# Optimization experiments

Measured on AMD Instinct MI355X. Metric: run time of the kernel, lower is better.

The kernel has to match this reference:

```python
import jax, jax.numpy as jnp
import numpy as np

N_USERS = 100000
M_ITEMS = 50000
D = 64
NNZ = 4_000_000
B = 4096
LAYERS = 3


def setup_inputs() -> dict:
    key = jax.random.key(0)
    ks = jax.random.split(key, 7)
    N = N_USERS + M_ITEMS
    return {
        "users": jax.random.randint(ks[0], (B,), 0, N_USERS, dtype=jnp.int64 if jax.config.jax_enable_x64 else jnp.int32),
        "items": jax.random.randint(ks[1], (B,), 0, M_ITEMS, dtype=jnp.int64 if jax.config.jax_enable_x64 else jnp.int32),
        "user_emb": jax.random.normal(ks[2], (N_USERS, D), dtype=jnp.float32) * 0.1,
        "item_emb": jax.random.normal(ks[3], (M_ITEMS, D), dtype=jnp.float32) * 0.1,
        "adj_rows": jax.random.randint(ks[4], (NNZ,), 0, N, dtype=jnp.int32),
        "adj_cols": jax.random.randint(ks[5], (NNZ,), 0, N, dtype=jnp.int32),
        "adj_vals": jax.random.uniform(ks[6], (NNZ,), dtype=jnp.float32),
    }


def reference(users, items, user_emb, item_emb, adj_rows, adj_cols, adj_vals):
    n_users = user_emb.shape[0]
    N = n_users + item_emb.shape[0]

    # computer(): multi-layer sparse propagation, mean over layer outputs
    all_emb = jnp.concatenate([user_emb, item_emb], axis=0)  # [N, D]
    acc = all_emb
    emb = all_emb
    for _ in range(LAYERS):
        # SpMM as gather + segment-sum: (A @ emb)[r] = sum_{e: row(e)=r} val(e) * emb[col(e)]
        messages = adj_vals[:, None] * emb[adj_cols]          # [NNZ, D]
        emb = jax.ops.segment_sum(messages, adj_rows, num_segments=N)
        acc = acc + emb
    light_out = acc / (LAYERS + 1)                            # mean over stacked layers

    all_users = light_out[:n_users]
    all_items = light_out[n_users:]

    # forward(users, items)
    u = all_users[users]                                      # [B, D]
    i = all_items[items]                                      # [B, D]
    gamma = jnp.sum(u * i, axis=1)                            # [B]
    return gamma
```

## Files before the change

### kernel.cpp

```cpp
#include <hip/hip_runtime.h>

#define N_USERS 100000
#define M_ITEMS 50000
#define N_TOTAL (N_USERS + M_ITEMS)
#define D 64
#define NNZ 4000000
#define BATCH 4096

#define RPB 128
#define BSHIFT 7
#define NBUCKETS ((N_TOTAL + RPB - 1) / RPB)
#define BCAP 7680

#define TILE 8192
#define SCAT_BLOCKS ((NNZ + TILE - 1) / TILE)
#define SCAT_THREADS 1024
#define EPT (TILE / SCAT_THREADS)
#define CPB 2

#define LS_THREADS 1024
#define LS_EPT 8

typedef __attribute__((ext_vector_type(2))) float f32x2;
typedef __attribute__((ext_vector_type(2))) int   i32x2;

__device__ __forceinline__ unsigned pack_bf16(float a, float b) {
    unsigned ua = __float_as_uint(a);
    unsigned ub = __float_as_uint(b);
    ua = (ua + 0x7FFFu + ((ua >> 16) & 1u)) >> 16;
    ub = (ub + 0x7FFFu + ((ub >> 16) & 1u)) & 0xFFFF0000u;
    return ua | ub;
}
__device__ __forceinline__ float bf16_lo(unsigned p) { return __uint_as_float(p << 16); }
__device__ __forceinline__ float bf16_hi(unsigned p) { return __uint_as_float(p & 0xFFFF0000u); }

__device__ __forceinline__ f32x2 unpack_bf16x2(unsigned p) {
    union { unsigned u[2]; f32x2 f; } r;
    r.u[0] = p << 16;
    r.u[1] = p & 0xFFFF0000u;
    return r.f;
}


__global__ void init_emb_kernel(const float4* __restrict__ ue,
                                const float4* __restrict__ ie,
                                uint2* __restrict__ emb) {
    size_t i = (size_t)blockIdx.x * blockDim.x + threadIdx.x;
    const size_t nu4  = (size_t)N_USERS * D / 4;
    const size_t tot4 = (size_t)N_TOTAL * D / 4;
    if (i >= tot4) return;
    float4 f = (i < nu4) ? ue[i] : ie[i - nu4];
    emb[i] = make_uint2(pack_bf16(f.x, f.y), pack_bf16(f.z, f.w));
}


__global__ void bucket_hist_kernel(const int* __restrict__ rows,
                                   int* __restrict__ bucketcnt) {
    __shared__ int h[NBUCKETS];
    for (int i = threadIdx.x; i < NBUCKETS; i += blockDim.x) h[i] = 0;
    __syncthreads();
    int stride = gridDim.x * blockDim.x;
    for (int e = blockIdx.x * blockDim.x + threadIdx.x; e < NNZ; e += stride)
        atomicAdd(&h[__builtin_nontemporal_load(rows + e) >> BSHIFT], 1);
    __syncthreads();
    for (int i = threadIdx.x; i < NBUCKETS; i += blockDim.x)
        if (h[i]) atomicAdd(&bucketcnt[i], h[i]);
}

__global__ void bucket_scan_kernel(const int* __restrict__ cnt,
                                   int* __restrict__ bucketoff,
                                   int* __restrict__ cursor) {
    __shared__ int sc[1024];
    int t = threadIdx.x;
    int i0 = t * 2, i1 = t * 2 + 1;
    int a = (i0 < NBUCKETS) ? cnt[i0] : 0;
    int b = (i1 < NBUCKETS) ? cnt[i1] : 0;
    sc[t] = a + b;
    __syncthreads();
    for (int o = 1; o < 1024; o <<= 1) {
        int v = (t >= o) ? sc[t - o] : 0;
        __syncthreads();
        sc[t] += v;
        __syncthreads();
    }
    int excl = (t == 0) ? 0 : sc[t - 1];
    if (i0 < NBUCKETS) { bucketoff[i0] = excl;     cursor[i0] = excl; }
    if (i1 < NBUCKETS) { bucketoff[i1] = excl + a; cursor[i1] = excl + a; }
    if (t == 0) bucketoff[NBUCKETS] = NNZ;
}

__global__ __launch_bounds__(SCAT_THREADS)
void bucket_scatter_kernel(const int* __restrict__ rows,
                           const int* __restrict__ cols,
                           const float* __restrict__ vals,
                           int* __restrict__ cursor,
                           int2* __restrict__ bucketed) {
    __shared__ int hist[NBUCKETS];
    __shared__ int loff[NBUCKETS + 1];
    __shared__ int partial[SCAT_THREADS];
    __shared__ int2 buf[TILE];
    __shared__ int dst[TILE];
    int t = threadIdx.x;
    size_t start = (size_t)blockIdx.x * TILE;
    int n = (int)(((size_t)NNZ - start < TILE) ? ((size_t)NNZ - start) : TILE);

    for (int i = t; i < NBUCKETS; i += SCAT_THREADS) hist[i] = 0;
    __syncthreads();
    int rowv[EPT];
    int rank[EPT];
#pragma unroll
    for (int k = 0; k < EPT; ++k) {
        int i = t + k * SCAT_THREADS;
        if (i < n) {
            int r = __builtin_nontemporal_load(rows + start + i);
            rowv[k] = r;
            rank[k] = atomicAdd(&hist[r >> BSHIFT], 1);
        }
    }
    __syncthreads();
    {
        int base = t * CPB;
        int s = 0;
#pragma unroll
        for (int j = 0; j < CPB; ++j) {
            int idx = base + j;
            if (idx < NBUCKETS) s += hist[idx];
        }
        partial[t] = s;
        __syncthreads();
        for (int o = 1; o < SCAT_THREADS; o <<= 1) {
            int v = (t >= o) ? partial[t - o] : 0;
            __syncthreads();
            partial[t] += v;
            __syncthreads();
        }
        int excl = (t == 0) ? 0 : partial[t - 1];
#pragma unroll
        for (int j = 0; j < CPB; ++j) {
            int idx = base + j;
            if (idx < NBUCKETS) { loff[idx] = excl; excl += hist[idx]; }
        }
        if (t == 0) loff[NBUCKETS] = n;
    }
    __syncthreads();
    for (int i = t; i < NBUCKETS; i += SCAT_THREADS) {
        int c = loff[i + 1] - loff[i];
        hist[i] = c ? atomicAdd(&cursor[i], c) : 0;
    }
    __syncthreads();
#pragma unroll
    for (int k = 0; k < EPT; ++k) {
        int i = t + k * SCAT_THREADS;
        if (i < n) {
            int r = rowv[k];
            int bkt = r >> BSHIFT;
            int slot = loff[bkt] + rank[k];
            int cv = __builtin_nontemporal_load(cols + start + i);
            float vv = __builtin_nontemporal_load(vals + start + i);
            buf[slot] = make_int2(((r & (RPB - 1)) << 18) | cv, __float_as_int(vv));
            dst[slot] = hist[bkt] + rank[k];
        }
    }
    __syncthreads();
    for (int i = t; i < n; i += SCAT_THREADS)
        bucketed[dst[i]] = buf[i];
}

__global__ __launch_bounds__(LS_THREADS)
void local_sort_kernel(const int* __restrict__ bucketoff,
                       const int2* __restrict__ bucketed,
                       int* __restrict__ row_start,
                       int2* __restrict__ edges) {
    __shared__ int hist[RPB];
    __shared__ int sc[RPB];
    __shared__ int2 buf[BCAP];
    int b = blockIdx.x;
    int t = threadIdx.x;
    int s = bucketoff[b], e = bucketoff[b + 1], n = e - s;

    if (t < RPB) hist[t] = 0;
    __syncthreads();
    int rl[LS_EPT], rank[LS_EPT];
    int2 pay[LS_EPT];
#pragma unroll
    for (int k = 0; k < LS_EPT; ++k) {
        int i = t + k * LS_THREADS;
        if (i < n) {
            i32x2 ev = __builtin_nontemporal_load((const i32x2*)(bucketed + s + i));
            rl[k] = (int)((unsigned)ev.x >> 18);
            pay[k] = make_int2((ev.x & 0x3FFFF) << 7, ev.y);
            rank[k] = atomicAdd(&hist[rl[k]], 1);
        }
    }
    __syncthreads();
    if (t < RPB) sc[t] = hist[t];
    __syncthreads();
    for (int o = 1; o < RPB; o <<= 1) {
        int v = (t < RPB && t >= o) ? sc[t - o] : 0;
        __syncthreads();
        if (t < RPB) sc[t] += v;
        __syncthreads();
    }
    if (t < RPB) {
        int excl = (t == 0) ? 0 : sc[t - 1];
        int gr = b * RPB + t;
        if (gr < N_TOTAL) row_start[gr] = s + excl;
    }
    if (b == 0 && t == 0) row_start[N_TOTAL] = NNZ;
    __syncthreads();
#pragma unroll
    for (int k = 0; k < LS_EPT; ++k) {
        int i = t + k * LS_THREADS;
        if (i < n) {
            int excl = (rl[k] == 0) ? 0 : sc[rl[k] - 1];
            int p = excl + rank[k];
            if (p < BCAP) buf[p] = pay[k];
            else          edges[s + p] = pay[k];
        }
    }
    __syncthreads();
    int m = (n < BCAP) ? n : BCAP;
    for (int i = t; i < m; i += LS_THREADS) edges[s + i] = buf[i];
}


#define EDGE_LD(p_) __builtin_nontemporal_load((const i32x2*)(p_))

#define EDGE_SLOT(ei, ji)                                                    \
    {                                                                        \
        int   c_  = (ji < n) ? ei.x : 0;                                     \
        float mv_ = (ji < n) ? __int_as_float(ei.y) : 0.0f;                  \
        uint4 p_  = *(const uint4*)(ebase + c_);                             \
        f32x2 vv_ = {mv_, mv_};                                              \
        a01 = __builtin_elementwise_fma(unpack_bf16x2(p_.x), vv_, a01);      \
        a23 = __builtin_elementwise_fma(unpack_bf16x2(p_.y), vv_, a23);      \
        a45 = __builtin_elementwise_fma(unpack_bf16x2(p_.z), vv_, a45);      \
        a67 = __builtin_elementwise_fma(unpack_bf16x2(p_.w), vv_, a67);      \
    }

#define SPMM_BODY(row_s, row_e)                                              \
    int n = (row_e) - (row_s);                                               \
    const int2* ep = edges + (row_s) + oct;                                  \
    f32x2 a01 = {0.f, 0.f}, a23 = {0.f, 0.f};                                \
    f32x2 a45 = {0.f, 0.f}, a67 = {0.f, 0.f};                                \
    int tmax = (n + 7) >> 3;                                                 \
    int t = 0;                                                               \
    for (; t + 4 <= tmax; t += 4) {                                          \
        i32x2 e0 = EDGE_LD(ep), e1 = EDGE_LD(ep + 8);                        \
        i32x2 e2 = EDGE_LD(ep + 16), e3 = EDGE_LD(ep + 24);                  \
        ep += 32;                                                            \
        int j0 = (t << 3) + oct;                                             \
        EDGE_SLOT(e0, j0);                                                   \
        EDGE_SLOT(e1, (j0 + 8));                                             \
        EDGE_SLOT(e2, (j0 + 16));                                            \
        EDGE_SLOT(e3, (j0 + 24));                                            \
    }                                                                        \
    if (t + 2 <= tmax) {                                                     \
        i32x2 e0 = EDGE_LD(ep), e1 = EDGE_LD(ep + 8);                        \
        ep += 16;                                                            \
        int j0 = (t << 3) + oct;                                             \
        EDGE_SLOT(e0, j0);                                                   \
        EDGE_SLOT(e1, (j0 + 8));                                             \
        t += 2;                                                              \
    }                                                                        \
    if (t < tmax) {                                                          \
        i32x2 e0 = EDGE_LD(ep);                                              \
        int j0 = (t << 3) + oct;                                             \
        EDGE_SLOT(e0, j0);                                                   \
    }                                                                        \
    _Pragma("unroll")                                                        \
    for (int o = 8; o <= 32; o <<= 1) {                                      \
        a01.x += __shfl_xor(a01.x, o, 64); a01.y += __shfl_xor(a01.y, o, 64);\
        a23.x += __shfl_xor(a23.x, o, 64); a23.y += __shfl_xor(a23.y, o, 64);\
        a45.x += __shfl_xor(a45.x, o, 64); a45.y += __shfl_xor(a45.y, o, 64);\
        a67.x += __shfl_xor(a67.x, o, 64); a67.y += __shfl_xor(a67.y, o, 64);\
    }

__global__ void spmm_csr_kernel(const int* __restrict__ row_start,
                                const int2* __restrict__ edges,
                                const char* __restrict__ emb_in,
                                uint4* __restrict__ emb_out) {
    int wave = (blockIdx.x * blockDim.x + threadIdx.x) >> 6;
    int lane = threadIdx.x & 63;
    if (wave >= N_TOTAL) return;
    int oct = lane >> 3;
    int ui  = lane & 7;
    const char* ebase = emb_in + (ui << 4);
    int s = row_start[wave];
    int e = row_start[wave + 1];
    SPMM_BODY(s, e);
    if (oct == 0)
        emb_out[(size_t)wave * 8 + ui] =
            make_uint4(pack_bf16(a01.x, a01.y), pack_bf16(a23.x, a23.y),
                       pack_bf16(a45.x, a45.y), pack_bf16(a67.x, a67.y));
}

__global__ void finalize_kernel(const int* __restrict__ users,
                                const int* __restrict__ items,
                                const float* __restrict__ ue,
                                const float* __restrict__ ie,
                                const int* __restrict__ row_start,
                                const int2* __restrict__ edges,
                                const char* __restrict__ embB,
                                const char* __restrict__ embA,
                                float* __restrict__ out) {
    int wave = (blockIdx.x * blockDim.x + threadIdx.x) >> 6;
    int lane = threadIdx.x & 63;
    if (wave >= BATCH) return;
    int oct = lane >> 3;
    int ui  = lane & 7;
    const char* ebase = embA + (ui << 4);

    int ru = users[wave];
    int ri = N_USERS + items[wave];

    f32x2 u01, u23, u45, u67, i01, i23, i45, i67;
    {
        SPMM_BODY(row_start[ru], row_start[ru + 1]);
        u01 = a01; u23 = a23; u45 = a45; u67 = a67;
    }
    {
        SPMM_BODY(row_start[ri], row_start[ri + 1]);
        i01 = a01; i23 = a23; i45 = a45; i67 = a67;
    }

    {
        const float4* up = (const float4*)(ue + (size_t)ru * D + 8 * ui);
        float4 f0 = up[0], f1 = up[1];
        u01 += (f32x2){f0.x, f0.y}; u23 += (f32x2){f0.z, f0.w};
        u45 += (f32x2){f1.x, f1.y}; u67 += (f32x2){f1.z, f1.w};
        uint4 pb = *(const uint4*)(embB + (size_t)ru * 128 + (ui << 4));
        uint4 pa = *(const uint4*)(embA + (size_t)ru * 128 + (ui << 4));
        u01 += unpack_bf16x2(pb.x) + unpack_bf16x2(pa.x);
        u23 += unpack_bf16x2(pb.y) + unpack_bf16x2(pa.y);
        u45 += unpack_bf16x2(pb.z) + unpack_bf16x2(pa.z);
        u67 += unpack_bf16x2(pb.w) + unpack_bf16x2(pa.w);
    }
    {
        const float4* ip = (const float4*)(ie + (size_t)items[wave] * D + 8 * ui);
        float4 f0 = ip[0], f1 = ip[1];
        i01 += (f32x2){f0.x, f0.y}; i23 += (f32x2){f0.z, f0.w};
        i45 += (f32x2){f1.x, f1.y}; i67 += (f32x2){f1.z, f1.w};
        uint4 pb = *(const uint4*)(embB + (size_t)ri * 128 + (ui << 4));
        uint4 pa = *(const uint4*)(embA + (size_t)ri * 128 + (ui << 4));
        i01 += unpack_bf16x2(pb.x) + unpack_bf16x2(pa.x);
        i23 += unpack_bf16x2(pb.y) + unpack_bf16x2(pa.y);
        i45 += unpack_bf16x2(pb.z) + unpack_bf16x2(pa.z);
        i67 += unpack_bf16x2(pb.w) + unpack_bf16x2(pa.w);
    }

    f32x2 d = u01 * i01;
    d = __builtin_elementwise_fma(u23, i23, d);
    d = __builtin_elementwise_fma(u45, i45, d);
    d = __builtin_elementwise_fma(u67, i67, d);
    float p = d.x + d.y;
#pragma unroll
    for (int o = 1; o <= 4; o <<= 1) p += __shfl_xor(p, o, 64);
    if (lane == 0) out[wave] = p * (1.0f / 16.0f);
}


extern "C" void kernel_launch(void* const* d_in, const int* in_sizes, int n_in,
                              void* d_out, int out_size, void* d_ws, size_t ws_size,
                              hipStream_t stream) {
    const int*   users = (const int*)d_in[0];
    const int*   items = (const int*)d_in[1];
    const float* ue    = (const float*)d_in[2];
    const float* ie    = (const float*)d_in[3];
    const int*   rows  = (const int*)d_in[4];
    const int*   cols  = (const int*)d_in[5];
    const float* vals  = (const float*)d_in[6];
    float*       out   = (float*)d_out;

    char* ws = (char*)d_ws;
    size_t off = 0;
    auto alloc = [&](size_t bytes) {
        void* p = ws + off;
        off += (bytes + 255) & ~(size_t)255;
        return p;
    };
    const size_t NBH = (size_t)N_TOTAL * D * sizeof(unsigned short);
    char*  embA      = (char*)alloc(NBH);
    char*  embB      = (char*)alloc(NBH);
    int*   row_start = (int*)alloc(((size_t)N_TOTAL + 1) * sizeof(int));
    int*   bucketcnt = (int*)alloc((size_t)NBUCKETS * sizeof(int));
    int*   bucketoff = (int*)alloc(((size_t)NBUCKETS + 1) * sizeof(int));
    int*   cursor    = (int*)alloc((size_t)NBUCKETS * sizeof(int));
    int2*  edges     = (int2*)alloc((size_t)NNZ * sizeof(int2) + 256);
    int2*  bucketed  = (int2*)alloc((size_t)NNZ * sizeof(int2));

    {
        size_t tot4 = (size_t)N_TOTAL * D / 4;
        init_emb_kernel<<<(unsigned)((tot4 + 255) / 256), 256, 0, stream>>>(
            (const float4*)ue, (const float4*)ie, (uint2*)embA);
    }

    hipMemsetAsync(bucketcnt, 0, (size_t)NBUCKETS * sizeof(int), stream);
    bucket_hist_kernel<<<512, 256, 0, stream>>>(rows, bucketcnt);
    bucket_scan_kernel<<<1, 1024, 0, stream>>>(bucketcnt, bucketoff, cursor);
    bucket_scatter_kernel<<<SCAT_BLOCKS, SCAT_THREADS, 0, stream>>>(
        rows, cols, vals, cursor, bucketed);
    local_sort_kernel<<<NBUCKETS, LS_THREADS, 0, stream>>>(
        bucketoff, bucketed, row_start, edges);

    spmm_csr_kernel<<<(N_TOTAL * 64 + 255) / 256, 256, 0, stream>>>(
        row_start, edges, embA, (uint4*)embB);

    spmm_csr_kernel<<<(N_TOTAL * 64 + 255) / 256, 256, 0, stream>>>(
        row_start, edges, embB, (uint4*)embA);

    finalize_kernel<<<(BATCH * 64 + 255) / 256, 256, 0, stream>>>(
        users, items, ue, ie, row_start, edges, embB, embA, out);
}
```

Measured before the change: 344.1 us.

## Sort edges within rows by column block to improve gather locality

The local sort now bins edges by (row, column>>12) rather than by row alone. Edges inside each row therefore come out ordered by coarse column block, which should improve cache locality of the embedding gathers in the SpMM. This needs a larger shared histogram and a 1024-wide block scan, and the shared staging buffer shrinks so more edges spill to direct global writes. The SpMM edge loads also switch from nontemporal loads to plain int2 loads.

```diff
diff --git a/kernel.cpp b/kernel.cpp
--- a/kernel.cpp
+++ b/kernel.cpp
@@ -10,7 +10,6 @@
 #define RPB 128
 #define BSHIFT 7
 #define NBUCKETS ((N_TOTAL + RPB - 1) / RPB)
-#define BCAP 7680
 
 #define TILE 8192
 #define SCAT_BLOCKS ((NNZ + TILE - 1) / TILE)
@@ -20,6 +19,11 @@
 
 #define LS_THREADS 1024
 #define LS_EPT 8
+#define CBSHIFT 12
+#define NCB 37
+#define NBINS (RPB * NCB)
+#define BPT ((NBINS + LS_THREADS - 1) / LS_THREADS)
+#define BCAP 4608
 
 typedef __attribute__((ext_vector_type(2))) float f32x2;
 typedef __attribute__((ext_vector_type(2))) int   i32x2;
@@ -31,8 +35,6 @@
     ub = (ub + 0x7FFFu + ((ub >> 16) & 1u)) & 0xFFFF0000u;
     return ua | ub;
 }
-__device__ __forceinline__ float bf16_lo(unsigned p) { return __uint_as_float(p << 16); }
-__device__ __forceinline__ float bf16_hi(unsigned p) { return __uint_as_float(p & 0xFFFF0000u); }
 
 __device__ __forceinline__ f32x2 unpack_bf16x2(unsigned p) {
     union { unsigned u[2]; f32x2 f; } r;
@@ -171,49 +173,65 @@
                        const int2* __restrict__ bucketed,
                        int* __restrict__ row_start,
                        int2* __restrict__ edges) {
-    __shared__ int hist[RPB];
-    __shared__ int sc[RPB];
+    __shared__ int hist[NBINS];
+    __shared__ int partial[LS_THREADS];
     __shared__ int2 buf[BCAP];
     int b = blockIdx.x;
     int t = threadIdx.x;
     int s = bucketoff[b], e = bucketoff[b + 1], n = e - s;
 
-    if (t < RPB) hist[t] = 0;
-    __syncthreads();
-    int rl[LS_EPT], rank[LS_EPT];
+    for (int i = t; i < NBINS; i += LS_THREADS) hist[i] = 0;
+    __syncthreads();
+    int binv[LS_EPT], rank[LS_EPT];
     int2 pay[LS_EPT];
 #pragma unroll
     for (int k = 0; k < LS_EPT; ++k) {
         int i = t + k * LS_THREADS;
         if (i < n) {
             i32x2 ev = __builtin_nontemporal_load((const i32x2*)(bucketed + s + i));
-            rl[k] = (int)((unsigned)ev.x >> 18);
-            pay[k] = make_int2((ev.x & 0x3FFFF) << 7, ev.y);
-            rank[k] = atomicAdd(&hist[rl[k]], 1);
-        }
-    }
-    __syncthreads();
-    if (t < RPB) sc[t] = hist[t];
-    __syncthreads();
-    for (int o = 1; o < RPB; o <<= 1) {
-        int v = (t < RPB && t >= o) ? sc[t - o] : 0;
+            int rl  = (int)((unsigned)ev.x >> 18);
+            int col = ev.x & 0x3FFFF;
+            binv[k] = rl * NCB + (col >> CBSHIFT);
+            pay[k] = make_int2(col << 7, ev.y);
+            rank[k] = atomicAdd(&hist[binv[k]], 1);
+        }
+    }
+    __syncthreads();
+    int loc[BPT];
+    {
+        int ssum = 0;
+#pragma unroll
+        for (int j = 0; j < BPT; ++j) {
+            int idx = t * BPT + j;
+            loc[j] = ssum;
+            if (idx < NBINS) ssum += hist[idx];
+        }
+        partial[t] = ssum;
         __syncthreads();
-        if (t < RPB) sc[t] += v;
-        __syncthreads();
-    }
+        for (int o = 1; o < LS_THREADS; o <<= 1) {
+            int v = (t >= o) ? partial[t - o] : 0;
+            __syncthreads();
+            partial[t] += v;
+            __syncthreads();
+        }
+        int excl = (t == 0) ? 0 : partial[t - 1];
+#pragma unroll
+        for (int j = 0; j < BPT; ++j) {
+            int idx = t * BPT + j;
+            if (idx < NBINS) hist[idx] = excl + loc[j];
+        }
+    }
+    __syncthreads();
     if (t < RPB) {
-        int excl = (t == 0) ? 0 : sc[t - 1];
         int gr = b * RPB + t;
-        if (gr < N_TOTAL) row_start[gr] = s + excl;
+        if (gr < N_TOTAL) row_start[gr] = s + hist[t * NCB];
     }
     if (b == 0 && t == 0) row_start[N_TOTAL] = NNZ;
-    __syncthreads();
 #pragma unroll
     for (int k = 0; k < LS_EPT; ++k) {
         int i = t + k * LS_THREADS;
         if (i < n) {
-            int excl = (rl[k] == 0) ? 0 : sc[rl[k] - 1];
-            int p = excl + rank[k];
+            int p = hist[binv[k]] + rank[k];
             if (p < BCAP) buf[p] = pay[k];
             else          edges[s + p] = pay[k];
         }
@@ -223,8 +241,6 @@
     for (int i = t; i < m; i += LS_THREADS) edges[s + i] = buf[i];
 }
 
-
-#define EDGE_LD(p_) __builtin_nontemporal_load((const i32x2*)(p_))
 
 #define EDGE_SLOT(ei, ji)                                                    \
     {                                                                        \
@@ -246,8 +262,7 @@
     int tmax = (n + 7) >> 3;                                                 \
     int t = 0;                                                               \
     for (; t + 4 <= tmax; t += 4) {                                          \
-        i32x2 e0 = EDGE_LD(ep), e1 = EDGE_LD(ep + 8);                        \
-        i32x2 e2 = EDGE_LD(ep + 16), e3 = EDGE_LD(ep + 24);                  \
+        int2 e0 = ep[0], e1 = ep[8], e2 = ep[16], e3 = ep[24];               \
         ep += 32;                                                            \
         int j0 = (t << 3) + oct;                                             \
         EDGE_SLOT(e0, j0);                                                   \
@@ -256,7 +271,7 @@
         EDGE_SLOT(e3, (j0 + 24));                                            \
     }                                                                        \
     if (t + 2 <= tmax) {                                                     \
-        i32x2 e0 = EDGE_LD(ep), e1 = EDGE_LD(ep + 8);                        \
+        int2 e0 = ep[0], e1 = ep[8];                                         \
         ep += 16;                                                            \
         int j0 = (t << 3) + oct;                                             \
         EDGE_SLOT(e0, j0);                                                   \
@@ -264,7 +279,7 @@
         t += 2;                                                              \
     }                                                                        \
     if (t < tmax) {                                                          \
-        i32x2 e0 = EDGE_LD(ep);                                              \
+        int2 e0 = ep[0];                                                     \
         int j0 = (t << 3) + oct;                                             \
         EDGE_SLOT(e0, j0);                                                   \
     }                                                                        \
```

Measured after the change: 345.9 us. About the same (+0.5%).

## Fuse first SpMM layer into local sort and merge init with histogram

Applied to the files above, without the earlier changes.

Runs the first propagation layer inside the per-bucket local sort kernel, reading edges from shared memory instead of reloading them from global memory, which saves one kernel launch and one pass over the edge array. Embedding init is merged with the bucket histogram into a single launch. Block scans now use wave shuffles instead of barrier-heavy shared-memory loops, and several output writes become nontemporal stores. The fused layer runs on only 16 waves per block of 128 rows, so it has less parallelism and latency hiding than the standalone SpMM kernel.

```diff
diff --git a/kernel.cpp b/kernel.cpp
--- a/kernel.cpp
+++ b/kernel.cpp
@@ -21,8 +21,26 @@
 #define LS_THREADS 1024
 #define LS_EPT 8
 
-typedef __attribute__((ext_vector_type(2))) float f32x2;
-typedef __attribute__((ext_vector_type(2))) int   i32x2;
+#define INIT_BLOCKS 9375
+#define HIST_BLOCKS 512
+
+typedef __attribute__((ext_vector_type(2))) float    f32x2;
+typedef __attribute__((ext_vector_type(2))) int      i32x2;
+typedef __attribute__((ext_vector_type(4))) unsigned u32x4;
+typedef __attribute__((ext_vector_type(2))) unsigned u32x2;
+
+__device__ __forceinline__ void nt_store_int2(int2 v, int2* p) {
+    i32x2 t; t.x = v.x; t.y = v.y;
+    __builtin_nontemporal_store(t, (i32x2*)p);
+}
+__device__ __forceinline__ void nt_store_uint4(uint4 v, uint4* p) {
+    u32x4 t; t.x = v.x; t.y = v.y; t.z = v.z; t.w = v.w;
+    __builtin_nontemporal_store(t, (u32x4*)p);
+}
+__device__ __forceinline__ void nt_store_uint2(uint2 v, uint2* p) {
+    u32x2 t; t.x = v.x; t.y = v.y;
+    __builtin_nontemporal_store(t, (u32x2*)p);
+}
 
 __device__ __forceinline__ unsigned pack_bf16(float a, float b) {
     unsigned ua = __float_as_uint(a);
@@ -31,8 +49,6 @@
     ub = (ub + 0x7FFFu + ((ub >> 16) & 1u)) & 0xFFFF0000u;
     return ua | ub;
 }
-__device__ __forceinline__ float bf16_lo(unsigned p) { return __uint_as_float(p << 16); }
-__device__ __forceinline__ float bf16_hi(unsigned p) { return __uint_as_float(p & 0xFFFF0000u); }
 
 __device__ __forceinline__ f32x2 unpack_bf16x2(unsigned p) {
     union { unsigned u[2]; f32x2 f; } r;
@@ -41,26 +57,47 @@
     return r.f;
 }
 
-
-__global__ void init_emb_kernel(const float4* __restrict__ ue,
-                                const float4* __restrict__ ie,
-                                uint2* __restrict__ emb) {
-    size_t i = (size_t)blockIdx.x * blockDim.x + threadIdx.x;
-    const size_t nu4  = (size_t)N_USERS * D / 4;
-    const size_t tot4 = (size_t)N_TOTAL * D / 4;
-    if (i >= tot4) return;
-    float4 f = (i < nu4) ? ue[i] : ie[i - nu4];
-    emb[i] = make_uint2(pack_bf16(f.x, f.y), pack_bf16(f.z, f.w));
-}
-
-
-__global__ void bucket_hist_kernel(const int* __restrict__ rows,
-                                   int* __restrict__ bucketcnt) {
+__device__ __forceinline__ int block_scan_incl_1024(int v, int* wsum) {
+    int lane = threadIdx.x & 63, wv = threadIdx.x >> 6;
+#pragma unroll
+    for (int o = 1; o < 64; o <<= 1) {
+        int u = __shfl_up(v, o, 64);
+        if (lane >= o) v += u;
+    }
+    if (lane == 63) wsum[wv] = v;
+    __syncthreads();
+    if (wv == 0) {
+        int w = (lane < 16) ? wsum[lane] : 0;
+#pragma unroll
+        for (int o = 1; o < 16; o <<= 1) {
+            int u = __shfl_up(w, o, 64);
+            if (lane >= o) w += u;
+        }
+        if (lane < 16) wsum[lane] = w;
+    }
+    __syncthreads();
+    return v + (wv ? wsum[wv - 1] : 0);
+}
+
+__global__ void init_hist_kernel(const float4* __restrict__ ue,
+                                 const float4* __restrict__ ie,
+                                 uint2* __restrict__ emb,
+                                 const int* __restrict__ rows,
+                                 int* __restrict__ bucketcnt) {
     __shared__ int h[NBUCKETS];
+    if (blockIdx.x < INIT_BLOCKS) {
+        size_t i = (size_t)blockIdx.x * 256 + threadIdx.x;
+        const size_t nu4 = (size_t)N_USERS * D / 4;
+        float4 f = (i < nu4) ? ue[i] : ie[i - nu4];
+        nt_store_uint2(make_uint2(pack_bf16(f.x, f.y), pack_bf16(f.z, f.w)),
+                       emb + i);
+        return;
+    }
+    int bid = blockIdx.x - INIT_BLOCKS;
     for (int i = threadIdx.x; i < NBUCKETS; i += blockDim.x) h[i] = 0;
     __syncthreads();
-    int stride = gridDim.x * blockDim.x;
-    for (int e = blockIdx.x * blockDim.x + threadIdx.x; e < NNZ; e += stride)
+    int stride = HIST_BLOCKS * 256;
+    for (int e = bid * 256 + threadIdx.x; e < NNZ; e += stride)
         atomicAdd(&h[__builtin_nontemporal_load(rows + e) >> BSHIFT], 1);
     __syncthreads();
     for (int i = threadIdx.x; i < NBUCKETS; i += blockDim.x)
@@ -70,20 +107,13 @@
 __global__ void bucket_scan_kernel(const int* __restrict__ cnt,
                                    int* __restrict__ bucketoff,
                                    int* __restrict__ cursor) {
-    __shared__ int sc[1024];
+    __shared__ int wsum[16];
     int t = threadIdx.x;
     int i0 = t * 2, i1 = t * 2 + 1;
     int a = (i0 < NBUCKETS) ? cnt[i0] : 0;
     int b = (i1 < NBUCKETS) ? cnt[i1] : 0;
-    sc[t] = a + b;
-    __syncthreads();
-    for (int o = 1; o < 1024; o <<= 1) {
-        int v = (t >= o) ? sc[t - o] : 0;
-        __syncthreads();
-        sc[t] += v;
-        __syncthreads();
-    }
-    int excl = (t == 0) ? 0 : sc[t - 1];
+    int incl = block_scan_incl_1024(a + b, wsum);
+    int excl = incl - a - b;
     if (i0 < NBUCKETS) { bucketoff[i0] = excl;     cursor[i0] = excl; }
     if (i1 < NBUCKETS) { bucketoff[i1] = excl + a; cursor[i1] = excl + a; }
     if (t == 0) bucketoff[NBUCKETS] = NNZ;
@@ -97,7 +127,7 @@
                            int2* __restrict__ bucketed) {
     __shared__ int hist[NBUCKETS];
     __shared__ int loff[NBUCKETS + 1];
-    __shared__ int partial[SCAT_THREADS];
+    __shared__ int wsum[16];
     __shared__ int2 buf[TILE];
     __shared__ int dst[TILE];
     int t = threadIdx.x;
@@ -126,15 +156,7 @@
             int idx = base + j;
             if (idx < NBUCKETS) s += hist[idx];
         }
-        partial[t] = s;
-        __syncthreads();
-        for (int o = 1; o < SCAT_THREADS; o <<= 1) {
-            int v = (t >= o) ? partial[t - o] : 0;
-            __syncthreads();
-            partial[t] += v;
-            __syncthreads();
-        }
-        int excl = (t == 0) ? 0 : partial[t - 1];
+        int excl = block_scan_incl_1024(s, wsum) - s;
 #pragma unroll
         for (int j = 0; j < CPB; ++j) {
             int idx = base + j;
@@ -163,14 +185,35 @@
     }
     __syncthreads();
     for (int i = t; i < n; i += SCAT_THREADS)
-        bucketed[dst[i]] = buf[i];
-}
+        nt_store_int2(buf[i], bucketed + dst[i]);
+}
+
+#define EDGE_SLOT2(ei)                                                       \
+    {                                                                        \
+        uint4 p_  = *(const uint4*)(ebase + (ei).x);                         \
+        f32x2 vv_ = {__int_as_float((ei).y), __int_as_float((ei).y)};        \
+        a01 = __builtin_elementwise_fma(unpack_bf16x2(p_.x), vv_, a01);      \
+        a23 = __builtin_elementwise_fma(unpack_bf16x2(p_.y), vv_, a23);      \
+        a45 = __builtin_elementwise_fma(unpack_bf16x2(p_.z), vv_, a45);      \
+        a67 = __builtin_elementwise_fma(unpack_bf16x2(p_.w), vv_, a67);      \
+    }
+
+#define ACC_BUTTERFLY()                                                      \
+    _Pragma("unroll")                                                        \
+    for (int o = 8; o <= 32; o <<= 1) {                                      \
+        a01.x += __shfl_xor(a01.x, o, 64); a01.y += __shfl_xor(a01.y, o, 64);\
+        a23.x += __shfl_xor(a23.x, o, 64); a23.y += __shfl_xor(a23.y, o, 64);\
+        a45.x += __shfl_xor(a45.x, o, 64); a45.y += __shfl_xor(a45.y, o, 64);\
+        a67.x += __shfl_xor(a67.x, o, 64); a67.y += __shfl_xor(a67.y, o, 64);\
+    }
 
 __global__ __launch_bounds__(LS_THREADS)
-void local_sort_kernel(const int* __restrict__ bucketoff,
-                       const int2* __restrict__ bucketed,
-                       int* __restrict__ row_start,
-                       int2* __restrict__ edges) {
+void local_sort_l1_kernel(const int* __restrict__ bucketoff,
+                          const int2* __restrict__ bucketed,
+                          int* __restrict__ row_start,
+                          int2* __restrict__ edges,
+                          const char* __restrict__ emb_in,
+                          uint4* __restrict__ emb_out) {
     __shared__ int hist[RPB];
     __shared__ int sc[RPB];
     __shared__ int2 buf[BCAP];
@@ -193,14 +236,19 @@
         }
     }
     __syncthreads();
-    if (t < RPB) sc[t] = hist[t];
-    __syncthreads();
-    for (int o = 1; o < RPB; o <<= 1) {
-        int v = (t < RPB && t >= o) ? sc[t - o] : 0;
-        __syncthreads();
-        if (t < RPB) sc[t] += v;
-        __syncthreads();
-    }
+    if (t < RPB) {
+        int lane = t & 63;
+        int v = hist[t];
+#pragma unroll
+        for (int o = 1; o < 64; o <<= 1) {
+            int u = __shfl_up(v, o, 64);
+            if (lane >= o) v += u;
+        }
+        sc[t] = v;
+    }
+    __syncthreads();
+    if (t >= 64 && t < RPB) sc[t] += sc[63];
+    __syncthreads();
     if (t < RPB) {
         int excl = (t == 0) ? 0 : sc[t - 1];
         int gr = b * RPB + t;
@@ -220,23 +268,43 @@
     }
     __syncthreads();
     int m = (n < BCAP) ? n : BCAP;
-    for (int i = t; i < m; i += LS_THREADS) edges[s + i] = buf[i];
-}
-
-
-#define EDGE_LD(p_) __builtin_nontemporal_load((const i32x2*)(p_))
-
-#define EDGE_SLOT(ei, ji)                                                    \
-    {                                                                        \
-        int   c_  = (ji < n) ? ei.x : 0;                                     \
-        float mv_ = (ji < n) ? __int_as_float(ei.y) : 0.0f;                  \
-        uint4 p_  = *(const uint4*)(ebase + c_);                             \
-        f32x2 vv_ = {mv_, mv_};                                              \
-        a01 = __builtin_elementwise_fma(unpack_bf16x2(p_.x), vv_, a01);      \
-        a23 = __builtin_elementwise_fma(unpack_bf16x2(p_.y), vv_, a23);      \
-        a45 = __builtin_elementwise_fma(unpack_bf16x2(p_.z), vv_, a45);      \
-        a67 = __builtin_elementwise_fma(unpack_bf16x2(p_.w), vv_, a67);      \
-    }
+    for (int i = t; i < m; i += LS_THREADS)
+        nt_store_int2(buf[i], edges + s + i);
+
+    int wv = t >> 6, lane = t & 63;
+    int oct = lane >> 3, ui = lane & 7;
+    const char* ebase = emb_in + (ui << 4);
+#define LEDGE(j_) (((j_) < nn) ? (((rs + (j_)) < BCAP) ? buf[rs + (j_)]      \
+                                 : edges[s + rs + (j_)]) : make_int2(0, 0))
+    for (int rr = 0; rr < 8; ++rr) {
+        int r = wv * 8 + rr;
+        int gr = b * RPB + r;
+        if (gr >= N_TOTAL) break;
+        int rs = (r == 0) ? 0 : sc[r - 1];
+        int nn = sc[r] - rs;
+        f32x2 a01 = {0.f, 0.f}, a23 = {0.f, 0.f};
+        f32x2 a45 = {0.f, 0.f}, a67 = {0.f, 0.f};
+        int tmax = (nn + 7) >> 3;
+        int tt = 0;
+        for (; tt + 4 <= tmax; tt += 4) {
+            int j0 = (tt << 3) + oct;
+            int2 e0 = LEDGE(j0), e1 = LEDGE(j0 + 8);
+            int2 e2 = LEDGE(j0 + 16), e3 = LEDGE(j0 + 24);
+            EDGE_SLOT2(e0); EDGE_SLOT2(e1); EDGE_SLOT2(e2); EDGE_SLOT2(e3);
+        }
+        for (; tt < tmax; ++tt) {
+            int2 e0 = LEDGE((tt << 3) + oct);
+            EDGE_SLOT2(e0);
+        }
+        ACC_BUTTERFLY();
+        if (oct == 0)
+            nt_store_uint4(
+                make_uint4(pack_bf16(a01.x, a01.y), pack_bf16(a23.x, a23.y),
+                           pack_bf16(a45.x, a45.y), pack_bf16(a67.x, a67.y)),
+                emb_out + (size_t)gr * 8 + ui);
+    }
+#undef LEDGE
+}
 
 #define SPMM_BODY(row_s, row_e)                                              \
     int n = (row_e) - (row_s);                                               \
@@ -246,35 +314,23 @@
     int tmax = (n + 7) >> 3;                                                 \
     int t = 0;                                                               \
     for (; t + 4 <= tmax; t += 4) {                                          \
-        i32x2 e0 = EDGE_LD(ep), e1 = EDGE_LD(ep + 8);                        \
-        i32x2 e2 = EDGE_LD(ep + 16), e3 = EDGE_LD(ep + 24);                  \
+        int j0 = (t << 3) + oct;                                             \
+        int2 e0 = ep[0], e1 = ep[8], e2 = ep[16], e3 = ep[24];               \
         ep += 32;                                                            \
+        if (j0      >= n) e0 = make_int2(0, 0);                              \
+        if (j0 + 8  >= n) e1 = make_int2(0, 0);                              \
+        if (j0 + 16 >= n) e2 = make_int2(0, 0);                              \
+        if (j0 + 24 >= n) e3 = make_int2(0, 0);                              \
+        EDGE_SLOT2(e0); EDGE_SLOT2(e1); EDGE_SLOT2(e2); EDGE_SLOT2(e3);      \
+    }                                                                        \
+    for (; t < tmax; ++t) {                                                  \
         int j0 = (t << 3) + oct;                                             \
-        EDGE_SLOT(e0, j0);                                                   \
-        EDGE_SLOT(e1, (j0 + 8));                                             \
-        EDGE_SLOT(e2, (j0 + 16));                                            \
-        EDGE_SLOT(e3, (j0 + 24));                                            \
+        int2 e0 = ep[0];                                                     \
+        ep += 8;                                                             \
+        if (j0 >= n) e0 = make_int2(0, 0);                                   \
+        EDGE_SLOT2(e0);                                                      \
     }                                                                        \
-    if (t + 2 <= tmax) {                                                     \
-        i32x2 e0 = EDGE_LD(ep), e1 = EDGE_LD(ep + 8);                        \
-        ep += 16;                                                            \
-        int j0 = (t << 3) + oct;                                             \
-        EDGE_SLOT(e0, j0);                                                   \
-        EDGE_SLOT(e1, (j0 + 8));                                             \
-        t += 2;                                                              \
-    }                                                                        \
-    if (t < tmax) {                                                          \
-        i32x2 e0 = EDGE_LD(ep);                                              \
-        int j0 = (t << 3) + oct;                                             \
-        EDGE_SLOT(e0, j0);                                                   \
-    }                                                                        \
-    _Pragma("unroll")                                                        \
-    for (int o = 8; o <= 32; o <<= 1) {                                      \
-        a01.x += __shfl_xor(a01.x, o, 64); a01.y += __shfl_xor(a01.y, o, 64);\
-        a23.x += __shfl_xor(a23.x, o, 64); a23.y += __shfl_xor(a23.y, o, 64);\
-        a45.x += __shfl_xor(a45.x, o, 64); a45.y += __shfl_xor(a45.y, o, 64);\
-        a67.x += __shfl_xor(a67.x, o, 64); a67.y += __shfl_xor(a67.y, o, 64);\
-    }
+    ACC_BUTTERFLY();
 
 __global__ void spmm_csr_kernel(const int* __restrict__ row_start,
                                 const int2* __restrict__ edges,
@@ -290,9 +346,10 @@
     int e = row_start[wave + 1];
     SPMM_BODY(s, e);
     if (oct == 0)
-        emb_out[(size_t)wave * 8 + ui] =
+        nt_store_uint4(
             make_uint4(pack_bf16(a01.x, a01.y), pack_bf16(a23.x, a23.y),
-                       pack_bf16(a45.x, a45.y), pack_bf16(a67.x, a67.y));
+                       pack_bf16(a45.x, a45.y), pack_bf16(a67.x, a67.y)),
+            emb_out + (size_t)wave * 8 + ui);
 }
 
 __global__ void finalize_kernel(const int* __restrict__ users,
@@ -389,22 +446,15 @@
     int2*  edges     = (int2*)alloc((size_t)NNZ * sizeof(int2) + 256);
     int2*  bucketed  = (int2*)alloc((size_t)NNZ * sizeof(int2));
 
-    {
-        size_t tot4 = (size_t)N_TOTAL * D / 4;
-        init_emb_kernel<<<(unsigned)((tot4 + 255) / 256), 256, 0, stream>>>(
-            (const float4*)ue, (const float4*)ie, (uint2*)embA);
-    }
-
     hipMemsetAsync(bucketcnt, 0, (size_t)NBUCKETS * sizeof(int), stream);
-    bucket_hist_kernel<<<512, 256, 0, stream>>>(rows, bucketcnt);
+    init_hist_kernel<<<INIT_BLOCKS + HIST_BLOCKS, 256, 0, stream>>>(
+        (const float4*)ue, (const float4*)ie, (uint2*)embA, rows, bucketcnt);
     bucket_scan_kernel<<<1, 1024, 0, stream>>>(bucketcnt, bucketoff, cursor);
     bucket_scatter_kernel<<<SCAT_BLOCKS, SCAT_THREADS, 0, stream>>>(
         rows, cols, vals, cursor, bucketed);
-    local_sort_kernel<<<NBUCKETS, LS_THREADS, 0, stream>>>(
-        bucketoff, bucketed, row_start, edges);
-
-    spmm_csr_kernel<<<(N_TOTAL * 64 + 255) / 256, 256, 0, stream>>>(
-        row_start, edges, embA, (uint4*)embB);
+
+    local_sort_l1_kernel<<<NBUCKETS, LS_THREADS, 0, stream>>>(
+        bucketoff, bucketed, row_start, edges, embA, (uint4*)embB);
 
     spmm_csr_kernel<<<(N_TOTAL * 64 + 255) / 256, 256, 0, stream>>>(
         row_start, edges, embB, (uint4*)embA);
```

Result: slower. 374.9 us (+8.9%).
